# Kernel optimization log

Hardware: AMD Instinct MI355X
Metric: run time of the kernel (lower is better)

## Reference

```python
import jax, jax.numpy as jnp
import numpy as np

N_NODES = 50000
N_EDGES = 800000
N_GRAPHS = 256
W_SCALE = 0.05  # keep activations bounded through 5 relu conv layers


def setup_inputs() -> dict:
    key = jax.random.key(0)
    ks = jax.random.split(key, 16)
    rn = lambda k, shape: W_SCALE * jax.random.normal(k, shape, dtype=jnp.float32)
    return {
        "x": jax.random.normal(ks[0], (N_NODES, 336), dtype=jnp.float32),
        "edge_index": jax.random.randint(ks[1], (2, N_EDGES), 0, N_NODES, dtype=jnp.int32),
        "batch": jnp.sort(jax.random.randint(ks[2], (N_NODES,), 0, N_GRAPHS, dtype=jnp.int32)),
        "w1_rel": rn(ks[3], (100, 336)),
        "w1_root": rn(ks[4], (100, 336)),
        "b1": rn(ks[5], (100,)),
        "w_rel": rn(ks[6], (4, 100, 100)),
        "w_root": rn(ks[7], (4, 100, 100)),
        "b": rn(ks[8], (4, 100)),
        "lw1": rn(ks[9], (100, 100)),
        "lb1": rn(ks[10], (100,)),
        "lw2": rn(ks[11], (100, 100)),
        "lb2": rn(ks[12], (100,)),
        "lw3": rn(ks[13], (29, 100)),
        "lb3": rn(ks[14], (29,)),
    }


def _graph_conv(x, edge_index, w_rel, w_root, bias):
    # PyG GraphConv: out_i = W_rel @ (sum_{j->i} x_j) + b + W_root @ x_i
    src, dst = edge_index[0], edge_index[1]
    agg = jax.ops.segment_sum(x[src], dst, num_segments=x.shape[0])  # [N, d_in]
    return agg @ w_rel.T + bias + x @ w_root.T


def reference(x, edge_index, batch, w1_rel, w1_root, b1, w_rel, w_root, b,
              lw1, lb1, lw2, lb2, lw3, lb3):
    h = jax.nn.relu(_graph_conv(x, edge_index, w1_rel, w1_root, b1))  # [N,100]
    for i in range(4):  # conv2..conv5 (structurally distinct params)
        h = jax.nn.relu(_graph_conv(h, edge_index, w_rel[i], w_root[i], b[i]))
    # global_mean_pool over graphs
    sums = jax.ops.segment_sum(h, batch, num_segments=N_GRAPHS)          # [G,100]
    counts = jax.ops.segment_sum(jnp.ones((h.shape[0],), h.dtype), batch,
                                 num_segments=N_GRAPHS)                  # [G]
    pooled = sums / jnp.maximum(counts, 1.0)[:, None]
    h = jax.nn.relu(pooled @ lw1.T + lb1)
    h = jax.nn.relu(h @ lw2.T + lb2)
    return h @ lw3.T + lb3  # [G, 29]
```

## Files before the change

### kernel.cpp

```cpp
#include <hip/hip_runtime.h>

#define N_NODES 50000
#define N_EDGES 800000
#define N_GRAPHS 256
#define F 100

#define SCAN_B 512
#define SCAN_NB 98
#define SCAN_PAD (SCAN_NB * SCAN_B)

#define PART_SZ 6250
#define FILL_CHUNK 2048

#define SROW 72
#define EPS 264

typedef __attribute__((ext_vector_type(8))) short bf16x8;
typedef __attribute__((ext_vector_type(4))) float f32x4;
typedef unsigned short ushort_t;
typedef unsigned int uint_t;

__device__ inline ushort_t f2bf(float f) {
  uint_t u = __float_as_uint(f);
  uint_t r = (u + 0x7fffu + ((u >> 16) & 1u)) >> 16;
  return (ushort_t)r;
}


__global__ __launch_bounds__(256) void hist_kernel(const int* __restrict__ dst,
                                                   int* __restrict__ cnt, int E) {
  int part = blockIdx.x & 7;
  int lo = part * PART_SZ, hi = lo + PART_SZ;
  int base = (blockIdx.x >> 3) * FILL_CHUNK;
  int end = base + FILL_CHUNK; if (end > E) end = E;
  for (int i = base + threadIdx.x; i < end; i += 256) {
    int d = dst[i];
    if (d >= lo && d < hi) atomicAdd(&cnt[d], 1);
  }
}

__global__ __launch_bounds__(SCAN_B) void scan1_kernel(const int* __restrict__ cnt,
                                                       int* __restrict__ excl,
                                                       int* __restrict__ bsum) {
  __shared__ int sh[SCAN_B];
  int t = threadIdx.x;
  int i = blockIdx.x * SCAN_B + t;
  int v = cnt[i];
  sh[t] = v;
  __syncthreads();
  for (int off = 1; off < SCAN_B; off <<= 1) {
    int u = (t >= off) ? sh[t - off] : 0;
    __syncthreads();
    sh[t] += u;
    __syncthreads();
  }
  excl[i] = sh[t] - v;
  if (t == SCAN_B - 1) bsum[blockIdx.x] = sh[t];
}

__global__ __launch_bounds__(128) void scan2_kernel(int* __restrict__ bsum) {
  __shared__ int sh[128];
  int t = threadIdx.x;
  int v = (t < SCAN_NB) ? bsum[t] : 0;
  sh[t] = v;
  __syncthreads();
  for (int off = 1; off < 128; off <<= 1) {
    int u = (t >= off) ? sh[t - off] : 0;
    __syncthreads();
    sh[t] += u;
    __syncthreads();
  }
  if (t < SCAN_NB) bsum[t] = sh[t] - v;
}

__global__ __launch_bounds__(SCAN_B) void scan3_kernel(const int* __restrict__ excl,
                                                       const int* __restrict__ bsum,
                                                       int* __restrict__ offs,
                                                       int* __restrict__ cursor) {
  int i = blockIdx.x * SCAN_B + threadIdx.x;
  int v = excl[i] + bsum[blockIdx.x];
  if (i <= N_NODES) { offs[i] = v; cursor[i] = v; }
}

__global__ __launch_bounds__(256) void fill_kernel(const int* __restrict__ src,
                                                   const int* __restrict__ dst,
                                                   int* __restrict__ cursor,
                                                   int* __restrict__ csr_src, int E) {
  int part = blockIdx.x & 7;
  int lo = part * PART_SZ, hi = lo + PART_SZ;
  int base = (blockIdx.x >> 3) * FILL_CHUNK;
  int end = base + FILL_CHUNK; if (end > E) end = E;
  for (int i = base + threadIdx.x; i < end; i += 256) {
    int d = dst[i];
    if (d >= lo && d < hi) {
      int p = atomicAdd(&cursor[d], 1);
      csr_src[p] = src[i];
    }
  }
}


__global__ void pack_w1_kernel(const float* __restrict__ w1_rel, const float* __restrict__ w1_root,
                               ushort_t* __restrict__ Wp1) {
  int row = blockIdx.x;
  for (int k = threadIdx.x; k < 384; k += 128) {
    float v = 0.f;
    if (k < 336) {
      if (row < 100) v = w1_rel[row * 336 + k];
      else if (row < 200) v = w1_root[(row - 100) * 336 + k];
    }
    Wp1[(size_t)row * 384 + k] = f2bf(v);
  }
}

__global__ void pack_w_kernel(const float* __restrict__ w_rel, const float* __restrict__ w_root,
                              ushort_t* __restrict__ Wp) {
  int row = blockIdx.x;
  int l = blockIdx.y;
  int k = threadIdx.x;
  float v = 0.f;
  if (k < 100) {
    if (row < 100) v = w_rel[((size_t)l * 100 + row) * 100 + k];
    else if (row < 200) v = w_root[((size_t)l * 100 + row - 100) * 100 + k];
  }
  Wp[((size_t)l * 208 + row) * 128 + k] = f2bf(v);
}


template <bool AF32>
__global__ __launch_bounds__(256) void conv_mfma(
    const void* __restrict__ Aptr, const ushort_t* __restrict__ Wp,
    const float* __restrict__ bias,
    ushort_t* __restrict__ ZP, int Kp) {
  __shared__ short smem[64 * SROW + 208 * SROW];
  __shared__ float bias_s[104];
  short* alds = smem;
  short* blds = smem + 64 * SROW;

  int tid = threadIdx.x;
  int n0 = blockIdx.x * 64;
  if (tid < 100) bias_s[tid] = bias[tid];

  f32x4 acc[13];
#pragma unroll
  for (int b = 0; b < 13; ++b) acc[b] = (f32x4)0.f;

  int w = tid >> 6, lane = tid & 63, q = lane >> 4, m16 = lane & 15;

  int ar[2], aq[2];
#pragma unroll
  for (int u = 0; u < 2; ++u) { int c = tid + u * 256; ar[u] = c >> 3; aq[u] = c & 7; }

  bf16x8 areg[2], breg[7];

  auto load_chunk = [&](int k0) {
#pragma unroll
    for (int u = 0; u < 2; ++u) {
      int node = n0 + ar[u];
      int k = k0 + aq[u] * 8;
      bf16x8 val = (bf16x8)0;
      if (AF32) {
        if (node < N_NODES && k < 336) {
          const float* p = (const float*)Aptr + (size_t)node * 336 + k;
          float4 f0 = *(const float4*)p;
          float4 f1 = *(const float4*)(p + 4);
          val[0] = (short)f2bf(f0.x); val[1] = (short)f2bf(f0.y);
          val[2] = (short)f2bf(f0.z); val[3] = (short)f2bf(f0.w);
          val[4] = (short)f2bf(f1.x); val[5] = (short)f2bf(f1.y);
          val[6] = (short)f2bf(f1.z); val[7] = (short)f2bf(f1.w);
        }
      } else {
        if (node < N_NODES)
          val = *(const bf16x8*)((const short*)Aptr + (size_t)node * 128 + k);
      }
      areg[u] = val;
    }
#pragma unroll
    for (int u = 0; u < 7; ++u) {
      int c = tid + u * 256;
      if (c < 1664) {
        int r = c >> 3, qq = c & 7;
        breg[u] = *(const bf16x8*)((const short*)Wp + (size_t)r * Kp + k0 + qq * 8);
      }
    }
  };

  load_chunk(0);

  for (int k0 = 0; k0 < Kp; k0 += 64) {
#pragma unroll
    for (int u = 0; u < 2; ++u)
      *(bf16x8*)&alds[ar[u] * SROW + aq[u] * 8] = areg[u];
#pragma unroll
    for (int u = 0; u < 7; ++u) {
      int c = tid + u * 256;
      if (c < 1664) {
        int r = c >> 3, qq = c & 7;
        *(bf16x8*)&blds[r * SROW + qq * 8] = breg[u];
      }
    }
    __syncthreads();
    if (k0 + 64 < Kp) load_chunk(k0 + 64);
#pragma unroll
    for (int s = 0; s < 2; ++s) {
      bf16x8 a = *(const bf16x8*)&alds[(w * 16 + m16) * SROW + s * 32 + q * 8];
#pragma unroll
      for (int b = 0; b < 13; ++b) {
        bf16x8 bf = *(const bf16x8*)&blds[(b * 16 + m16) * SROW + s * 32 + q * 8];
        acc[b] = __builtin_amdgcn_mfma_f32_16x16x32_bf16(a, bf, acc[b], 0, 0, 0);
      }
    }
    __syncthreads();
  }

  short* ep = smem;
#pragma unroll
  for (int b = 0; b < 13; ++b) {
    int n = b * 16 + m16;
    if (n < 200) {
      int c = (n < 100) ? n : (n + 28);
      float add = (n < 100) ? 0.f : bias_s[(n - 100) & 127];
#pragma unroll
      for (int r = 0; r < 4; ++r) {
        int row = w * 16 + q * 4 + r;
        ep[row * EPS + c] = (short)f2bf(acc[b][r] + add);
      }
    }
  }
  __syncthreads();
#pragma unroll
  for (int j = 0; j < 8; ++j) {
    int i = tid + j * 256;
    int row = i >> 5, c16 = i & 31;
    int node = n0 + row;
    if (node < N_NODES) {
      *(uint4*)(ZP + (size_t)node * 256 + c16 * 8) =
          *(const uint4*)&ep[row * EPS + c16 * 8];
    }
  }
}


__global__ __launch_bounds__(256) void gather_bf16(
    const ushort_t* __restrict__ ZP,
    const int* __restrict__ offs, const int* __restrict__ csr,
    ushort_t* __restrict__ H) {
  int node = blockIdx.x * 4 + (threadIdx.x >> 6);
  node = __builtin_amdgcn_readfirstlane(node);
  int lane = threadIdx.x & 63;
  int off = (lane < 50 ? lane : 49) * 2;

  uint_t z = *(const uint_t*)(ZP + (size_t)node * 256 + 128 + off);
  float p0[8], p1[8];
#pragma unroll
  for (int u = 0; u < 8; ++u) { p0[u] = 0.f; p1[u] = 0.f; }
  p0[0] = __uint_as_float(z << 16);
  p1[0] = __uint_as_float(z & 0xffff0000u);

  int s = offs[node], e = offs[node + 1];
  for (int j = s; j < e; j += 64) {
    int take = e - j; if (take > 64) take = 64;
    int vidx = (lane < take) ? csr[j + lane] : 0;
    int u = 0;
    for (; u + 8 <= take; u += 8) {
      uint_t zz[8];
#pragma unroll
      for (int t = 0; t < 8; ++t) {
        int idx = __builtin_amdgcn_readlane(vidx, u + t);
        zz[t] = *(const uint_t*)(ZP + (size_t)idx * 256 + off);
      }
#pragma unroll
      for (int t = 0; t < 8; ++t) {
        p0[t] += __uint_as_float(zz[t] << 16);
        p1[t] += __uint_as_float(zz[t] & 0xffff0000u);
      }
    }
    int cnt = take - u;
    if (cnt > 0) {
      uint_t zz[7];
#pragma unroll
      for (int t = 0; t < 7; ++t) {
        if (t < cnt) {
          int idx = __builtin_amdgcn_readlane(vidx, u + t);
          zz[t] = *(const uint_t*)(ZP + (size_t)idx * 256 + off);
        }
      }
#pragma unroll
      for (int t = 0; t < 7; ++t) {
        if (t < cnt) {
          p0[t] += __uint_as_float(zz[t] << 16);
          p1[t] += __uint_as_float(zz[t] & 0xffff0000u);
        }
      }
    }
  }
  float a0 = ((p0[0] + p0[1]) + (p0[2] + p0[3])) + ((p0[4] + p0[5]) + (p0[6] + p0[7]));
  float a1 = ((p1[0] + p1[1]) + (p1[2] + p1[3])) + ((p1[4] + p1[5]) + (p1[6] + p1[7]));
  a0 = fmaxf(a0, 0.f);
  a1 = fmaxf(a1, 0.f);
  uint_t outp = (uint_t)f2bf(a0) | ((uint_t)f2bf(a1) << 16);
  if (lane >= 50) outp = 0u;
  *(uint_t*)(H + (size_t)node * 128 + lane * 2) = outp;
}


__global__ __launch_bounds__(1024) void pool_kernel(const ushort_t* __restrict__ H,
                                                    const int* __restrict__ batch,
                                                    float* __restrict__ pooled) {
  int g = blockIdx.x;
  int t = threadIdx.x;
  int lo = 0, hi = N_NODES;
  while (lo < hi) { int mid = (lo + hi) >> 1; if (batch[mid] < g) lo = mid + 1; else hi = mid; }
  int s = lo;
  hi = N_NODES;
  while (lo < hi) { int mid = (lo + hi) >> 1; if (batch[mid] <= g) lo = mid + 1; else hi = mid; }
  int e = lo;

  int row = t >> 6;
  int lane = t & 63;
  int off = (lane < 50 ? lane : 49) * 2;
  float a0 = 0.f, a1 = 0.f;
  for (int n = s + row; n < e; n += 16) {
    uint_t z = *(const uint_t*)(H + (size_t)n * 128 + off);
    a0 += __uint_as_float(z << 16);
    a1 += __uint_as_float(z & 0xffff0000u);
  }
  __shared__ float sh[16][104];
  if (lane < 50) { sh[row][lane * 2] = a0; sh[row][lane * 2 + 1] = a1; }
  __syncthreads();
  if (t < 100) {
    float acc = 0.f;
#pragma unroll
    for (int r = 0; r < 16; ++r) acc += sh[r][t];
    int cnt = e - s;
    float d = (cnt > 0) ? (float)cnt : 1.f;
    pooled[(size_t)g * F + t] = acc / d;
  }
}


__global__ void mlp_kernel(const float* __restrict__ pooled,
                           const float* __restrict__ lw1, const float* __restrict__ lb1,
                           const float* __restrict__ lw2, const float* __restrict__ lb2,
                           const float* __restrict__ lw3, const float* __restrict__ lb3,
                           float* __restrict__ out) {
  int g = blockIdx.x;
  int t = threadIdx.x;
  __shared__ float r0[F], r1[F], r2[F];
  if (t < F) r0[t] = pooled[(size_t)g * F + t];
  __syncthreads();
  if (t < F) {
    float s = lb1[t];
    for (int k = 0; k < F; ++k) s += r0[k] * lw1[t * F + k];
    r1[t] = fmaxf(s, 0.f);
  }
  __syncthreads();
  if (t < F) {
    float s = lb2[t];
    for (int k = 0; k < F; ++k) s += r1[k] * lw2[t * F + k];
    r2[t] = fmaxf(s, 0.f);
  }
  __syncthreads();
  if (t < 29) {
    float s = lb3[t];
    for (int k = 0; k < F; ++k) s += r2[k] * lw3[t * F + k];
    out[g * 29 + t] = s;
  }
}


extern "C" void kernel_launch(void* const* d_in, const int* in_sizes, int n_in,
                              void* d_out, int out_size, void* d_ws, size_t ws_size,
                              hipStream_t stream) {
  const float* x       = (const float*)d_in[0];
  const int*   ei      = (const int*)d_in[1];
  const int*   batch   = (const int*)d_in[2];
  const float* w1_rel  = (const float*)d_in[3];
  const float* w1_root = (const float*)d_in[4];
  const float* b1      = (const float*)d_in[5];
  const float* w_rel   = (const float*)d_in[6];
  const float* w_root  = (const float*)d_in[7];
  const float* bvec    = (const float*)d_in[8];
  const float* lw1     = (const float*)d_in[9];
  const float* lb1     = (const float*)d_in[10];
  const float* lw2     = (const float*)d_in[11];
  const float* lb2     = (const float*)d_in[12];
  const float* lw3     = (const float*)d_in[13];
  const float* lb3     = (const float*)d_in[14];
  float* out = (float*)d_out;

  char* ws = (char*)d_ws;
  size_t o = 0;
  auto alloc = [&](size_t bytes) { void* p = ws + o; o = (o + bytes + 511) & ~(size_t)511; return p; };
  ushort_t* H    = (ushort_t*)alloc((size_t)N_NODES * 128 * 2);
  ushort_t* ZP   = (ushort_t*)alloc((size_t)N_NODES * 256 * 2);
  ushort_t* Wp1  = (ushort_t*)alloc((size_t)208 * 384 * 2);
  ushort_t* Wp   = (ushort_t*)alloc((size_t)4 * 208 * 128 * 2);
  float*    pooled = (float*)alloc((size_t)N_GRAPHS * F * 4);
  int* cnt    = (int*)alloc((size_t)SCAN_PAD * 4);
  int* excl   = (int*)alloc((size_t)SCAN_PAD * 4);
  int* bsum   = (int*)alloc((size_t)128 * 4);
  int* offs   = (int*)alloc((size_t)(N_NODES + 1) * 4);
  int* cursor = (int*)alloc((size_t)(N_NODES + 1) * 4);
  int* csr    = (int*)alloc((size_t)N_EDGES * 4);

  const int E = N_EDGES;
  const int* srcv = ei;
  const int* dstv = ei + E;

  int nchunk = (E + FILL_CHUNK - 1) / FILL_CHUNK;
  hipMemsetAsync(cnt, 0, (size_t)SCAN_PAD * sizeof(int), stream);
  hist_kernel<<<nchunk * 8, 256, 0, stream>>>(dstv, cnt, E);
  scan1_kernel<<<SCAN_NB, SCAN_B, 0, stream>>>(cnt, excl, bsum);
  scan2_kernel<<<1, 128, 0, stream>>>(bsum);
  scan3_kernel<<<SCAN_NB, SCAN_B, 0, stream>>>(excl, bsum, offs, cursor);
  fill_kernel<<<nchunk * 8, 256, 0, stream>>>(srcv, dstv, cursor, csr, E);

  pack_w1_kernel<<<208, 128, 0, stream>>>(w1_rel, w1_root, Wp1);
  pack_w_kernel<<<dim3(208, 4), 128, 0, stream>>>(w_rel, w_root, Wp);

  int mmgrid = (N_NODES + 63) / 64;
  conv_mfma<true><<<mmgrid, 256, 0, stream>>>(x, Wp1, b1, ZP, 384);
  gather_bf16<<<N_NODES / 4, 256, 0, stream>>>(ZP, offs, csr, H);
  for (int l = 0; l < 4; ++l) {
    conv_mfma<false><<<mmgrid, 256, 0, stream>>>(H, Wp + (size_t)l * 208 * 128,
                                                 bvec + (size_t)l * F, ZP, 128);
    gather_bf16<<<N_NODES / 4, 256, 0, stream>>>(ZP, offs, csr, H);
  }
  pool_kernel<<<N_GRAPHS, 1024, 0, stream>>>(H, batch, pooled);
  mlp_kernel<<<N_GRAPHS, 128, 0, stream>>>(pooled, lw1, lb1, lw2, lb2, lw3, lb3, out);
}
```

Baseline: 456.7 us.

## Add persistent register-fragment MFMA kernel for 100x100 conv layers

```diff
diff --git a/kernel.cpp b/kernel.cpp
--- a/kernel.cpp
+++ b/kernel.cpp
@@ -236,6 +236,75 @@
     if (node < N_NODES) {
       *(uint4*)(ZP + (size_t)node * 256 + c16 * 8) =
           *(const uint4*)&ep[row * EPS + c16 * 8];
+    }
+  }
+}
+
+
+__global__ __launch_bounds__(256) void conv_reg(
+    const ushort_t* __restrict__ A,
+    const ushort_t* __restrict__ Wp,
+    const float* __restrict__ bias,
+    ushort_t* __restrict__ ZP) {
+  __shared__ short bl[13 * 4 * 64 * 8];
+  __shared__ __align__(16) float bias_s[104];
+
+  int tid = threadIdx.x;
+  if (tid < 100) bias_s[tid] = bias[tid];
+
+#pragma unroll
+  for (int u = 0; u < 13; ++u) {
+    int i = tid + u * 256;
+    int fr = i >> 6, lp = i & 63;
+    int b = fr >> 2, s = fr & 3;
+    int qq = lp >> 4, mm = lp & 15;
+    *(bf16x8*)&bl[(size_t)i * 8] =
+        *(const bf16x8*)(Wp + (size_t)(b * 16 + mm) * 128 + s * 32 + qq * 8);
+  }
+  __syncthreads();
+
+  int w = tid >> 6, lane = tid & 63, q = lane >> 4, m16 = lane & 15;
+  int nwaves = gridDim.x * 4;
+  int gw = blockIdx.x * 4 + w;
+
+  for (int tile = gw; tile < 3125; tile += nwaves) {
+    int m0 = tile * 16;
+    const ushort_t* ap = A + (size_t)(m0 + m16) * 128 + q * 8;
+    bf16x8 a0 = *(const bf16x8*)(ap);
+    bf16x8 a1 = *(const bf16x8*)(ap + 32);
+    bf16x8 a2 = *(const bf16x8*)(ap + 64);
+    bf16x8 a3 = *(const bf16x8*)(ap + 96);
+
+    f32x4 acc[13];
+#pragma unroll
+    for (int b = 0; b < 13; ++b) acc[b] = (f32x4)0.f;
+
+#pragma unroll
+    for (int s = 0; s < 4; ++s) {
+      bf16x8 a = (s == 0) ? a0 : (s == 1) ? a1 : (s == 2) ? a2 : a3;
+#pragma unroll
+      for (int b = 0; b < 13; ++b) {
+        bf16x8 bf = *(const bf16x8*)&bl[((b * 4 + s) * 64 + lane) * 8];
+        acc[b] = __builtin_amdgcn_mfma_f32_16x16x32_bf16(bf, a, acc[b], 0, 0, 0);
+      }
+    }
+
+    size_t zbase = (size_t)(m0 + m16) * 256;
+#pragma unroll
+    for (int b = 0; b < 13; ++b) {
+      int n0 = b * 16 + q * 4;
+      if (n0 < 100) {
+        ushort4 v;
+        v.x = f2bf(acc[b][0]); v.y = f2bf(acc[b][1]);
+        v.z = f2bf(acc[b][2]); v.w = f2bf(acc[b][3]);
+        *(ushort4*)(ZP + zbase + n0) = v;
+      } else if (n0 < 200) {
+        float4 bb = *(const float4*)&bias_s[n0 - 100];
+        ushort4 v;
+        v.x = f2bf(acc[b][0] + bb.x); v.y = f2bf(acc[b][1] + bb.y);
+        v.z = f2bf(acc[b][2] + bb.z); v.w = f2bf(acc[b][3] + bb.w);
+        *(ushort4*)(ZP + zbase + n0 + 28) = v;
+      }
     }
   }
 }
@@ -423,8 +492,8 @@
   conv_mfma<true><<<mmgrid, 256, 0, stream>>>(x, Wp1, b1, ZP, 384);
   gather_bf16<<<N_NODES / 4, 256, 0, stream>>>(ZP, offs, csr, H);
   for (int l = 0; l < 4; ++l) {
-    conv_mfma<false><<<mmgrid, 256, 0, stream>>>(H, Wp + (size_t)l * 208 * 128,
-                                                 bvec + (size_t)l * F, ZP, 128);
+    conv_reg<<<512, 256, 0, stream>>>(H, Wp + (size_t)l * 208 * 128,
+                                      bvec + (size_t)l * F, ZP);
     gather_bf16<<<N_NODES / 4, 256, 0, stream>>>(ZP, offs, csr, H);
   }
   pool_kernel<<<N_GRAPHS, 1024, 0, stream>>>(H, batch, pooled);
```

After: 456.5 us. Within noise of the previous version (-0.0%).

## Fuse aggregation and GEMM for layers 2-5 into one aggregate-first kernel

Applied to the files above, without the earlier changes.

```diff
diff --git a/kernel.cpp b/kernel.cpp
--- a/kernel.cpp
+++ b/kernel.cpp
@@ -14,6 +14,7 @@
 
 #define SROW 72
 #define EPS 264
+#define AST 264
 
 typedef __attribute__((ext_vector_type(8))) short bf16x8;
 typedef __attribute__((ext_vector_type(4))) float f32x4;
@@ -113,17 +114,17 @@
   }
 }
 
-__global__ void pack_w_kernel(const float* __restrict__ w_rel, const float* __restrict__ w_root,
-                              ushort_t* __restrict__ Wp) {
-  int row = blockIdx.x;
-  int l = blockIdx.y;
+__global__ void pack_wf_kernel(const float* __restrict__ w_rel, const float* __restrict__ w_root,
+                               ushort_t* __restrict__ Wf) {
+  int rowl = blockIdx.x;
+  int l = rowl >> 7, row = rowl & 127;
   int k = threadIdx.x;
   float v = 0.f;
-  if (k < 100) {
-    if (row < 100) v = w_rel[((size_t)l * 100 + row) * 100 + k];
-    else if (row < 200) v = w_root[((size_t)l * 100 + row - 100) * 100 + k];
-  }
-  Wp[((size_t)l * 208 + row) * 128 + k] = f2bf(v);
+  if (row < 100) {
+    if (k < 100) v = w_rel[((size_t)l * 100 + row) * 100 + k];
+    else if (k >= 128 && k < 228) v = w_root[((size_t)l * 100 + row) * 100 + (k - 128)];
+  }
+  Wf[(size_t)rowl * 256 + k] = f2bf(v);
 }
 
 
@@ -301,6 +302,99 @@
   uint_t outp = (uint_t)f2bf(a0) | ((uint_t)f2bf(a1) << 16);
   if (lane >= 50) outp = 0u;
   *(uint_t*)(H + (size_t)node * 128 + lane * 2) = outp;
+}
+
+
+__global__ __launch_bounds__(512) void fused_layer(
+    const ushort_t* __restrict__ Hin,
+    const ushort_t* __restrict__ Wf,
+    const float* __restrict__ bias,
+    const int* __restrict__ offs, const int* __restrict__ csr,
+    ushort_t* __restrict__ Hout) {
+  __shared__ short alds[16 * AST];
+
+  int tid = threadIdx.x;
+  int w = tid >> 6, lane = tid & 63, q = lane >> 4, m16 = lane & 15;
+  int tile = blockIdx.x;
+
+  for (int sub = 0; sub < 2; ++sub) {
+    int row = w * 2 + sub;
+    int node = tile * 16 + row;
+    node = __builtin_amdgcn_readfirstlane(node);
+    uint_t hv = *(const uint_t*)(Hin + (size_t)node * 128 + lane * 2);
+    *(uint_t*)&alds[row * AST + 128 + lane * 2] = hv;
+    int off = (lane < 50 ? lane : 49) * 2;
+    float p0[8], p1[8];
+#pragma unroll
+    for (int u = 0; u < 8; ++u) { p0[u] = 0.f; p1[u] = 0.f; }
+    int s = offs[node], e = offs[node + 1];
+    for (int j = s; j < e; j += 64) {
+      int take = e - j; if (take > 64) take = 64;
+      int vidx = (lane < take) ? csr[j + lane] : 0;
+      int u = 0;
+      for (; u + 8 <= take; u += 8) {
+        uint_t zz[8];
+#pragma unroll
+        for (int t = 0; t < 8; ++t) {
+          int idx = __builtin_amdgcn_readlane(vidx, u + t);
+          zz[t] = *(const uint_t*)(Hin + (size_t)idx * 128 + off);
+        }
+#pragma unroll
+        for (int t = 0; t < 8; ++t) {
+          p0[t] += __uint_as_float(zz[t] << 16);
+          p1[t] += __uint_as_float(zz[t] & 0xffff0000u);
+        }
+      }
+      int cnt = take - u;
+      if (cnt > 0) {
+        uint_t zz[7];
+#pragma unroll
+        for (int t = 0; t < 7; ++t) {
+          if (t < cnt) {
+            int idx = __builtin_amdgcn_readlane(vidx, u + t);
+            zz[t] = *(const uint_t*)(Hin + (size_t)idx * 128 + off);
+          }
+        }
+#pragma unroll
+        for (int t = 0; t < 7; ++t) {
+          if (t < cnt) {
+            p0[t] += __uint_as_float(zz[t] << 16);
+            p1[t] += __uint_as_float(zz[t] & 0xffff0000u);
+          }
+        }
+      }
+    }
+    float a0 = ((p0[0] + p0[1]) + (p0[2] + p0[3])) + ((p0[4] + p0[5]) + (p0[6] + p0[7]));
+    float a1 = ((p1[0] + p1[1]) + (p1[2] + p1[3])) + ((p1[4] + p1[5]) + (p1[6] + p1[7]));
+    uint_t outp = (uint_t)f2bf(a0) | ((uint_t)f2bf(a1) << 16);
+    if (lane >= 50) outp = 0u;
+    *(uint_t*)&alds[row * AST + lane * 2] = outp;
+  }
+
+  bf16x8 wreg[8];
+#pragma unroll
+  for (int s = 0; s < 8; ++s)
+    wreg[s] = *(const bf16x8*)(Wf + (size_t)(w * 16 + m16) * 256 + s * 32 + q * 8);
+  int n0 = w * 16 + q * 4;
+  float4 bb = make_float4(0.f, 0.f, 0.f, 0.f);
+  if (n0 < 100) bb = *(const float4*)(bias + n0);
+
+  __syncthreads();
+
+  f32x4 acc = (f32x4)0.f;
+#pragma unroll
+  for (int s = 0; s < 8; ++s) {
+    bf16x8 af = *(const bf16x8*)&alds[m16 * AST + s * 32 + q * 8];
+    acc = __builtin_amdgcn_mfma_f32_16x16x32_bf16(wreg[s], af, acc, 0, 0, 0);
+  }
+
+  int node = tile * 16 + m16;
+  ushort4 v;
+  v.x = f2bf(fmaxf(acc[0] + bb.x, 0.f));
+  v.y = f2bf(fmaxf(acc[1] + bb.y, 0.f));
+  v.z = f2bf(fmaxf(acc[2] + bb.z, 0.f));
+  v.w = f2bf(fmaxf(acc[3] + bb.w, 0.f));
+  *(ushort4*)(Hout + (size_t)node * 128 + n0) = v;
 }
 
 
@@ -392,10 +486,11 @@
   char* ws = (char*)d_ws;
   size_t o = 0;
   auto alloc = [&](size_t bytes) { void* p = ws + o; o = (o + bytes + 511) & ~(size_t)511; return p; };
-  ushort_t* H    = (ushort_t*)alloc((size_t)N_NODES * 128 * 2);
+  ushort_t* H1   = (ushort_t*)alloc((size_t)N_NODES * 128 * 2);
+  ushort_t* H2   = (ushort_t*)alloc((size_t)N_NODES * 128 * 2);
   ushort_t* ZP   = (ushort_t*)alloc((size_t)N_NODES * 256 * 2);
   ushort_t* Wp1  = (ushort_t*)alloc((size_t)208 * 384 * 2);
-  ushort_t* Wp   = (ushort_t*)alloc((size_t)4 * 208 * 128 * 2);
+  ushort_t* Wf   = (ushort_t*)alloc((size_t)4 * 128 * 256 * 2);
   float*    pooled = (float*)alloc((size_t)N_GRAPHS * F * 4);
   int* cnt    = (int*)alloc((size_t)SCAN_PAD * 4);
   int* excl   = (int*)alloc((size_t)SCAN_PAD * 4);
@@ -417,16 +512,19 @@
   fill_kernel<<<nchunk * 8, 256, 0, stream>>>(srcv, dstv, cursor, csr, E);
 
   pack_w1_kernel<<<208, 128, 0, stream>>>(w1_rel, w1_root, Wp1);
-  pack_w_kernel<<<dim3(208, 4), 128, 0, stream>>>(w_rel, w_root, Wp);
+  pack_wf_kernel<<<512, 256, 0, stream>>>(w_rel, w_root, Wf);
 
   int mmgrid = (N_NODES + 63) / 64;
   conv_mfma<true><<<mmgrid, 256, 0, stream>>>(x, Wp1, b1, ZP, 384);
-  gather_bf16<<<N_NODES / 4, 256, 0, stream>>>(ZP, offs, csr, H);
+  gather_bf16<<<N_NODES / 4, 256, 0, stream>>>(ZP, offs, csr, H1);
+
+  const ushort_t* hin = H1;
+  ushort_t* hout = H2;
   for (int l = 0; l < 4; ++l) {
-    conv_mfma<false><<<mmgrid, 256, 0, stream>>>(H, Wp + (size_t)l * 208 * 128,
-                                                 bvec + (size_t)l * F, ZP, 128);
-    gather_bf16<<<N_NODES / 4, 256, 0, stream>>>(ZP, offs, csr, H);
-  }
-  pool_kernel<<<N_GRAPHS, 1024, 0, stream>>>(H, batch, pooled);
+    fused_layer<<<N_NODES / 16, 512, 0, stream>>>(hin, Wf + (size_t)l * 128 * 256,
+                                                  bvec + (size_t)l * F, offs, csr, hout);
+    const ushort_t* tmp = hout; hout = (ushort_t*)hin; hin = tmp;
+  }
+  pool_kernel<<<N_GRAPHS, 1024, 0, stream>>>(hin, batch, pooled);
   mlp_kernel<<<N_GRAPHS, 128, 0, stream>>>(pooled, lw1, lb1, lw2, lb2, lw3, lb3, out);
 }
```

Result: no change. 457.0 us (+0.1%).
